# Optimization experiments

Measured on AMD Instinct MI355X. Metric: run time of the kernel, lower is better.

Reference implementation:

```python
import jax, jax.numpy as jnp
import numpy as np

B, C, H, W = 64, 256, 32, 32


def setup_inputs() -> dict:
    key = jax.random.key(0)
    ks = jax.random.split(key, 7)
    x1 = jax.random.normal(ks[0], (B, C, H, W), dtype=jnp.float32)
    x2 = jax.random.normal(ks[1], (B, C, H, W), dtype=jnp.float32)
    # 1x1 Conv2d(C+1 -> C, bias=False): weight squeezed to (C, C+1)
    conv_w = jax.random.normal(ks[2], (C, C + 1), dtype=jnp.float32) * (1.0 / np.sqrt(C + 1))
    # caLayer: Conv1d(2->4, k=1) + ReLU + Conv1d(4->1, k=1) + Softmax(dim=1)
    ca_w1 = jax.random.normal(ks[3], (4, 2), dtype=jnp.float32) * (1.0 / np.sqrt(2))
    ca_b1 = jax.random.normal(ks[4], (4,), dtype=jnp.float32) * 0.1
    ca_w2 = jax.random.normal(ks[5], (1, 4), dtype=jnp.float32) * 0.5
    ca_b2 = jax.random.normal(ks[6], (1,), dtype=jnp.float32) * 0.1
    return {"x1": x1, "x2": x2, "conv_w": conv_w, "ca_w1": ca_w1,
            "ca_b1": ca_b1, "ca_w2": ca_w2, "ca_b2": ca_b2}


def _branch_pool(x, conv_w):
    # x: (B, C, H, W)
    b, c, h, w = x.shape
    center = x[:, :, h // 2, w // 2][:, :, None, None]          # (B, C, 1, 1)
    dot = jnp.sum(x * center, axis=1, keepdims=True) / c        # (B, 1, H, W)
    concatenated = jnp.concatenate([x, dot], axis=1)            # (B, C+1, H, W)
    attn = jax.nn.sigmoid(jnp.einsum('oc,bchw->bohw', conv_w, concatenated))
    norm = attn / (jnp.sum(attn, axis=(2, 3), keepdims=True) + 1e-8)
    return jnp.sum(x * norm, axis=(2, 3))                       # (B, C)


def reference(x1, x2, conv_w, ca_w1, ca_b1, ca_w2, ca_b2):
    pooled = jnp.stack([_branch_pool(x1, conv_w),
                        _branch_pool(x2, conv_w)], axis=1)      # (B, 2, C)
    # caLayer: kernel-size-1 Conv1d == channel-mixing matmul over axis 1
    h1 = jax.nn.relu(jnp.einsum('oi,bic->boc', ca_w1, pooled) + ca_b1[None, :, None])
    h2 = jnp.einsum('oi,bic->boc', ca_w2, h1) + ca_b2[None, :, None]  # (B, 1, C)
    x_weights = jax.nn.softmax(h2, axis=1)                      # softmax over size-1 dim
    y_total = pooled * x_weights                                # broadcast (B,2,C)
    return jnp.sum(y_total, axis=1)                             # (B, C)
```

## Files before the change

kernel.cpp:

```cpp
#include <hip/hip_runtime.h>
#include <hip/hip_bf16.h>
#include <math.h>

typedef __bf16 bf16x8 __attribute__((ext_vector_type(8)));
typedef float  f32x16 __attribute__((ext_vector_type(16)));

#define WLAST_OFF 32768
#define CEN_OFF   33024
#define ACCA_OFF  65792
#define ACCX_OFF  98560

static __device__ __forceinline__ unsigned f2bf_u(float f) {
    unsigned u = __builtin_bit_cast(unsigned, f);
    return (u + 0x7fffu + ((u >> 16) & 1u)) >> 16;
}
static __device__ __forceinline__ unsigned pkbf(float a, float b) {
    __hip_bfloat162 h = __float22bfloat162_rn(make_float2(a, b));
    unsigned u; __builtin_memcpy(&u, &h, 4); return u;
}

template<int CTRL, int RM>
static __device__ __forceinline__ float dpp_add(float x) {
    int yi = __builtin_amdgcn_update_dpp(0, __builtin_bit_cast(int, x), CTRL, RM, 0xF, true);
    return x + __builtin_bit_cast(float, yi);
}
static __device__ __forceinline__ float red32(float x) {
    x = dpp_add<0x121, 0xF>(x);
    x = dpp_add<0x122, 0xF>(x);
    x = dpp_add<0x124, 0xF>(x);
    x = dpp_add<0x128, 0xF>(x);
    x = dpp_add<0x142, 0xA>(x);
    return x;
}

static __device__ __forceinline__ int swz(int hwr) {
    return ((hwr >> 2) & 7) << 2;
}

__global__ void k_init(const float* __restrict__ x1, const float* __restrict__ x2,
                       const float* __restrict__ conv_w, float* __restrict__ ws) {
    int bk = blockIdx.x;
    int tid = threadIdx.x;
    if (bk < 256) {
        int idx = bk * 256 + tid;
        int j  = idx & 7;
        int l  = (idx >> 3) & 63;
        int ot = (idx >> 9) & 7;
        int S  = idx >> 12;
        int o  = ot * 32 + (l & 31);
        int k  = S * 16 + (l >> 5) * 8 + j;
        ((unsigned short*)ws)[idx] = (unsigned short)f2bf_u(conv_w[o * 257 + k]);
        if (idx < 256) ws[WLAST_OFF + idx] = conv_w[idx * 257 + 256];
        ws[ACCA_OFF + idx] = 0.0f;
    } else {
        int xb = bk - 256;
        const float* xp = ((xb < 64) ? x1 : x2) + (size_t)(xb & 63) * (256 * 1024);
        ws[CEN_OFF + xb * 256 + tid] = xp[(size_t)tid * 1024 + 528];
    }
}

__global__ __launch_bounds__(256, 4)
void k_main(const float* __restrict__ x1, const float* __restrict__ x2,
            float* __restrict__ ws) {
    int bx = blockIdx.x;
    int xb = blockIdx.y;
    const float* xp = ((xb < 64) ? x1 : x2) + (size_t)(xb & 63) * (256 * 1024);
    const unsigned short* wfrag = (const unsigned short*)ws;
    float* accA = ws + ACCA_OFF + xb * 256;
    float* accX = ws + ACCX_OFF + xb * 256;
    int hw0 = bx * 64;

    int tid = threadIdx.x;
    int l = tid & 63, w = tid >> 6;
    int lw = l & 31, q = l >> 5;

    __shared__ unsigned sx[64][128];
    __shared__ float sd[64][17];
    __shared__ float scen[256];
    __shared__ float swl[256];
    __shared__ float dotf[64];

    int hwi = tid & 15, kc = tid >> 4;

    float cenv = ws[CEN_OFF + xb * 256 + tid];
    float wlv  = ws[WLAST_OFF + tid];
    const float* xst = xp + (size_t)(kc * 2) * 1024 + hw0 + hwi * 4;
    float4 xv[16];
    #pragma unroll
    for (int s = 0; s < 8; ++s) {
        xv[2 * s]     = *(const float4*)(xst + (size_t)(32 * s) * 1024);
        xv[2 * s + 1] = *(const float4*)(xst + (size_t)(32 * s + 1) * 1024);
    }
    __builtin_amdgcn_sched_barrier(0);
    scen[tid] = cenv;
    swl[tid]  = wlv;
    __syncthreads();

    float dotp[4] = {0.f, 0.f, 0.f, 0.f};
    #pragma unroll
    for (int s = 0; s < 8; ++s) {
        float4 e = xv[2 * s], o4 = xv[2 * s + 1];
        int c = kc * 2 + 32 * s;
        float s0 = scen[c], s1 = scen[c + 1];
        dotp[0] += e.x * s0 + o4.x * s1;
        dotp[1] += e.y * s0 + o4.y * s1;
        dotp[2] += e.z * s0 + o4.z * s1;
        dotp[3] += e.w * s0 + o4.w * s1;
        int col = kc + 16 * s;
        float ee[4] = {e.x, e.y, e.z, e.w};
        float oo[4] = {o4.x, o4.y, o4.z, o4.w};
        #pragma unroll
        for (int j = 0; j < 4; ++j) {
            int jj = (hwi + j) & 3;
            int hwr = hwi * 4 + jj;
            sx[hwr][col ^ swz(hwr)] = pkbf(ee[jj], oo[jj]);
        }
    }
    #pragma unroll
    for (int j = 0; j < 4; ++j) sd[hwi * 4 + j][kc] = dotp[j];
    __syncthreads();

    if (tid < 64) {
        float ssum = 0.f;
        #pragma unroll
        for (int k2 = 0; k2 < 16; ++k2) ssum += sd[tid][k2];
        dotf[tid] = ssum * (1.0f / 256.0f);
    }

    f32x16 acc[2][2];
    #pragma unroll
    for (int i = 0; i < 2; ++i)
        #pragma unroll
        for (int j = 0; j < 2; ++j)
            #pragma unroll
            for (int e = 0; e < 16; ++e) acc[i][j][e] = 0.0f;

    auto loadA = [&](int S, int it) -> bf16x8 {
        return *(const bf16x8*)(wfrag + (size_t)((S * 8 + (w * 2 + it)) * 64 + l) * 8);
    };
    auto loadB = [&](int S, int jt) -> bf16x8 {
        int hwr = jt * 32 + lw;
        int colb = (S * 8 + q * 4) ^ swz(hwr);
        bf16x8 r; __builtin_memcpy(&r, &sx[hwr][colb], 16);
        return r;
    };

    bf16x8 A0[2], A1[2], A2[2];
    A0[0] = loadA(0, 0); A0[1] = loadA(0, 1);
    A1[0] = loadA(1, 0); A1[1] = loadA(1, 1);
    #pragma unroll
    for (int S = 0; S < 16; ++S) {
        bf16x8 b0 = loadB(S, 0);
        bf16x8 b1 = loadB(S, 1);
        if (S + 2 < 16) { A2[0] = loadA(S + 2, 0); A2[1] = loadA(S + 2, 1); }
        acc[0][0] = __builtin_amdgcn_mfma_f32_32x32x16_bf16(A0[0], b0, acc[0][0], 0, 0, 0);
        acc[0][1] = __builtin_amdgcn_mfma_f32_32x32x16_bf16(A0[0], b1, acc[0][1], 0, 0, 0);
        acc[1][0] = __builtin_amdgcn_mfma_f32_32x32x16_bf16(A0[1], b0, acc[1][0], 0, 0, 0);
        acc[1][1] = __builtin_amdgcn_mfma_f32_32x32x16_bf16(A0[1], b1, acc[1][1], 0, 0, 0);
        A0[0] = A1[0]; A0[1] = A1[1];
        A1[0] = A2[0]; A1[1] = A2[1];
    }
    __syncthreads();

    float dv0 = dotf[lw];
    float dv1 = dotf[32 + lw];
    #pragma unroll
    for (int it = 0; it < 2; ++it) {
        int ob = w * 64 + it * 32;
        #pragma unroll
        for (int r = 0; r < 16; ++r) {
            int row = (r & 3) + 8 * (r >> 2) + 4 * q;
            int o = ob + row;
            float wl = swl[o];
            float z0 = acc[it][0][r] + wl * dv0;
            float z1 = acc[it][1][r] + wl * dv1;
            float a0 = __builtin_amdgcn_rcpf(1.0f + __expf(-z0));
            float a1 = __builtin_amdgcn_rcpf(1.0f + __expf(-z1));
            int col = o >> 1;
            unsigned w0 = sx[lw][col ^ swz(lw)];
            unsigned w1 = sx[32 + lw][col ^ swz(32 + lw)];
            float xv0, xv1;
            if (o & 1) {
                xv0 = __builtin_bit_cast(float, w0 & 0xffff0000u);
                xv1 = __builtin_bit_cast(float, w1 & 0xffff0000u);
            } else {
                xv0 = __builtin_bit_cast(float, w0 << 16);
                xv1 = __builtin_bit_cast(float, w1 << 16);
            }
            float sA = red32(a0 + a1);
            float sX = red32(a0 * xv0 + a1 * xv1);
            if (lw == 31) {
                atomicAdd(&accA[o], sA);
                atomicAdd(&accX[o], sX);
            }
        }
    }
}

__global__ void k_out(const float* __restrict__ ws, float* __restrict__ out) {
    int idx = blockIdx.x * 256 + threadIdx.x;
    int b = idx >> 8, o = idx & 255;
    float a0 = ws[ACCA_OFF + b * 256 + o];
    float p0 = ws[ACCX_OFF + b * 256 + o];
    float a1 = ws[ACCA_OFF + (64 + b) * 256 + o];
    float p1 = ws[ACCX_OFF + (64 + b) * 256 + o];
    out[idx] = p0 / (a0 + 1e-8f) + p1 / (a1 + 1e-8f);
}

extern "C" void kernel_launch(void* const* d_in, const int* in_sizes, int n_in,
                              void* d_out, int out_size, void* d_ws, size_t ws_size,
                              hipStream_t stream) {
    const float* x1     = (const float*)d_in[0];
    const float* x2     = (const float*)d_in[1];
    const float* conv_w = (const float*)d_in[2];
    float* ws  = (float*)d_ws;
    float* out = (float*)d_out;

    k_init<<<384, 256, 0, stream>>>(x1, x2, conv_w, ws);
    k_main<<<dim3(16, 128), 256, 0, stream>>>(x1, x2, ws);
    k_out<<<64, 256, 0, stream>>>(ws, out);
}
```

Measured before the change: 184.0 us.

## Split main kernel across 512 threads with per-slab LDS layout

Doubles the block to 512 threads (8 waves), so each thread loads half as many x values and each wave computes a single 32-row output tile (two MFMA accumulators instead of four). The LDS staging of x is reorganised into [S][hw][8] slabs with a simpler XOR swizzle, and the center vector is read straight from global memory instead of through shared memory. Partial dot products are reduced with wave shuffles before being written to LDS. The aim is more latency hiding and less register pressure per thread, at the cost of extra waves per block and an A-fragment prefetch depth of one.

```diff
diff --git a/kernel.cpp b/kernel.cpp
--- a/kernel.cpp
+++ b/kernel.cpp
@@ -31,10 +31,6 @@
     x = dpp_add<0x128, 0xF>(x);
     x = dpp_add<0x142, 0xA>(x);
     return x;
-}
-
-static __device__ __forceinline__ int swz(int hwr) {
-    return ((hwr >> 2) & 7) << 2;
 }
 
 __global__ void k_init(const float* __restrict__ x1, const float* __restrict__ x2,
@@ -59,7 +55,7 @@
     }
 }
 
-__global__ __launch_bounds__(256, 4)
+__global__ __launch_bounds__(512, 6)
 void k_main(const float* __restrict__ x1, const float* __restrict__ x2,
             float* __restrict__ ws) {
     int bx = blockIdx.x;
@@ -71,128 +67,123 @@
     int hw0 = bx * 64;
 
     int tid = threadIdx.x;
-    int l = tid & 63, w = tid >> 6;
+    int w = tid >> 6;
+    int l = tid & 63;
     int lw = l & 31, q = l >> 5;
 
-    __shared__ unsigned sx[64][128];
-    __shared__ float sd[64][17];
-    __shared__ float scen[256];
+    __shared__ __align__(16) unsigned sx[16][64][8];
+    __shared__ float sd[64][9];
     __shared__ float swl[256];
     __shared__ float dotf[64];
 
     int hwi = tid & 15, kc = tid >> 4;
 
-    float cenv = ws[CEN_OFF + xb * 256 + tid];
-    float wlv  = ws[WLAST_OFF + tid];
+    if (tid < 256) swl[tid] = ws[WLAST_OFF + tid];
+
+    const float* cenp = ws + CEN_OFF + xb * 256;
+    float2 cv[4];
+    #pragma unroll
+    for (int s = 0; s < 4; ++s)
+        cv[s] = *(const float2*)(cenp + kc * 2 + 64 * s);
     const float* xst = xp + (size_t)(kc * 2) * 1024 + hw0 + hwi * 4;
-    float4 xv[16];
-    #pragma unroll
-    for (int s = 0; s < 8; ++s) {
-        xv[2 * s]     = *(const float4*)(xst + (size_t)(32 * s) * 1024);
-        xv[2 * s + 1] = *(const float4*)(xst + (size_t)(32 * s + 1) * 1024);
+    float4 xv[8];
+    #pragma unroll
+    for (int s = 0; s < 4; ++s) {
+        xv[2 * s]     = *(const float4*)(xst + (size_t)(64 * s) * 1024);
+        xv[2 * s + 1] = *(const float4*)(xst + (size_t)(64 * s + 1) * 1024);
     }
     __builtin_amdgcn_sched_barrier(0);
-    scen[tid] = cenv;
-    swl[tid]  = wlv;
-    __syncthreads();
 
     float dotp[4] = {0.f, 0.f, 0.f, 0.f};
     #pragma unroll
-    for (int s = 0; s < 8; ++s) {
+    for (int s = 0; s < 4; ++s) {
         float4 e = xv[2 * s], o4 = xv[2 * s + 1];
-        int c = kc * 2 + 32 * s;
-        float s0 = scen[c], s1 = scen[c + 1];
+        float s0 = cv[s].x, s1 = cv[s].y;
         dotp[0] += e.x * s0 + o4.x * s1;
         dotp[1] += e.y * s0 + o4.y * s1;
         dotp[2] += e.z * s0 + o4.z * s1;
         dotp[3] += e.w * s0 + o4.w * s1;
-        int col = kc + 16 * s;
+        int S  = (kc >> 3) + 4 * s;
+        int wd = kc & 7;
         float ee[4] = {e.x, e.y, e.z, e.w};
         float oo[4] = {o4.x, o4.y, o4.z, o4.w};
         #pragma unroll
         for (int j = 0; j < 4; ++j) {
-            int jj = (hwi + j) & 3;
+            int jj  = (hwi + j) & 3;
             int hwr = hwi * 4 + jj;
-            sx[hwr][col ^ swz(hwr)] = pkbf(ee[jj], oo[jj]);
+            sx[S][hwr][wd ^ (((hwr >> 4) & 1) << 2)] = pkbf(ee[jj], oo[jj]);
         }
     }
     #pragma unroll
-    for (int j = 0; j < 4; ++j) sd[hwi * 4 + j][kc] = dotp[j];
+    for (int j = 0; j < 4; ++j) {
+        float v = dotp[j];
+        v += __shfl_xor(v, 16, 64);
+        v += __shfl_xor(v, 32, 64);
+        dotp[j] = v;
+    }
+    if (l < 16) {
+        #pragma unroll
+        for (int j = 0; j < 4; ++j) sd[hwi * 4 + j][w] = dotp[j];
+    }
     __syncthreads();
 
     if (tid < 64) {
         float ssum = 0.f;
         #pragma unroll
-        for (int k2 = 0; k2 < 16; ++k2) ssum += sd[tid][k2];
+        for (int k2 = 0; k2 < 8; ++k2) ssum += sd[tid][k2];
         dotf[tid] = ssum * (1.0f / 256.0f);
     }
 
-    f32x16 acc[2][2];
-    #pragma unroll
-    for (int i = 0; i < 2; ++i)
-        #pragma unroll
-        for (int j = 0; j < 2; ++j)
-            #pragma unroll
-            for (int e = 0; e < 16; ++e) acc[i][j][e] = 0.0f;
-
-    auto loadA = [&](int S, int it) -> bf16x8 {
-        return *(const bf16x8*)(wfrag + (size_t)((S * 8 + (w * 2 + it)) * 64 + l) * 8);
-    };
-    auto loadB = [&](int S, int jt) -> bf16x8 {
-        int hwr = jt * 32 + lw;
-        int colb = (S * 8 + q * 4) ^ swz(hwr);
-        bf16x8 r; __builtin_memcpy(&r, &sx[hwr][colb], 16);
-        return r;
-    };
-
-    bf16x8 A0[2], A1[2], A2[2];
-    A0[0] = loadA(0, 0); A0[1] = loadA(0, 1);
-    A1[0] = loadA(1, 0); A1[1] = loadA(1, 1);
+    f32x16 acc[2];
+    #pragma unroll
+    for (int e = 0; e < 16; ++e) { acc[0][e] = 0.0f; acc[1][e] = 0.0f; }
+
+    int sig = ((lw >> 4) & 1) << 2;
+    const unsigned* b0p = &sx[0][lw][(q * 4) ^ sig];
+    const unsigned* b1p = &sx[0][32 + lw][(q * 4) ^ sig];
+    const unsigned short* ap = wfrag + (size_t)(w * 64 + l) * 8;
+
+    bf16x8 a0 = *(const bf16x8*)(ap);
     #pragma unroll
     for (int S = 0; S < 16; ++S) {
-        bf16x8 b0 = loadB(S, 0);
-        bf16x8 b1 = loadB(S, 1);
-        if (S + 2 < 16) { A2[0] = loadA(S + 2, 0); A2[1] = loadA(S + 2, 1); }
-        acc[0][0] = __builtin_amdgcn_mfma_f32_32x32x16_bf16(A0[0], b0, acc[0][0], 0, 0, 0);
-        acc[0][1] = __builtin_amdgcn_mfma_f32_32x32x16_bf16(A0[0], b1, acc[0][1], 0, 0, 0);
-        acc[1][0] = __builtin_amdgcn_mfma_f32_32x32x16_bf16(A0[1], b0, acc[1][0], 0, 0, 0);
-        acc[1][1] = __builtin_amdgcn_mfma_f32_32x32x16_bf16(A0[1], b1, acc[1][1], 0, 0, 0);
-        A0[0] = A1[0]; A0[1] = A1[1];
-        A1[0] = A2[0]; A1[1] = A2[1];
+        bf16x8 a1;
+        if (S + 1 < 16) a1 = *(const bf16x8*)(ap + (size_t)(S + 1) * 4096);
+        bf16x8 b0, b1;
+        __builtin_memcpy(&b0, b0p + S * 512, 16);
+        __builtin_memcpy(&b1, b1p + S * 512, 16);
+        acc[0] = __builtin_amdgcn_mfma_f32_32x32x16_bf16(a0, b0, acc[0], 0, 0, 0);
+        acc[1] = __builtin_amdgcn_mfma_f32_32x32x16_bf16(a0, b1, acc[1], 0, 0, 0);
+        a0 = a1;
     }
     __syncthreads();
 
     float dv0 = dotf[lw];
     float dv1 = dotf[32 + lw];
     #pragma unroll
-    for (int it = 0; it < 2; ++it) {
-        int ob = w * 64 + it * 32;
-        #pragma unroll
-        for (int r = 0; r < 16; ++r) {
-            int row = (r & 3) + 8 * (r >> 2) + 4 * q;
-            int o = ob + row;
-            float wl = swl[o];
-            float z0 = acc[it][0][r] + wl * dv0;
-            float z1 = acc[it][1][r] + wl * dv1;
-            float a0 = __builtin_amdgcn_rcpf(1.0f + __expf(-z0));
-            float a1 = __builtin_amdgcn_rcpf(1.0f + __expf(-z1));
-            int col = o >> 1;
-            unsigned w0 = sx[lw][col ^ swz(lw)];
-            unsigned w1 = sx[32 + lw][col ^ swz(32 + lw)];
-            float xv0, xv1;
-            if (o & 1) {
-                xv0 = __builtin_bit_cast(float, w0 & 0xffff0000u);
-                xv1 = __builtin_bit_cast(float, w1 & 0xffff0000u);
-            } else {
-                xv0 = __builtin_bit_cast(float, w0 << 16);
-                xv1 = __builtin_bit_cast(float, w1 << 16);
-            }
-            float sA = red32(a0 + a1);
-            float sX = red32(a0 * xv0 + a1 * xv1);
-            if (lw == 31) {
-                atomicAdd(&accA[o], sA);
-                atomicAdd(&accX[o], sX);
-            }
+    for (int r = 0; r < 16; ++r) {
+        int row = (r & 3) + 8 * (r >> 2) + 4 * q;
+        int o = w * 32 + row;
+        float wl = swl[o];
+        float z0 = acc[0][r] + wl * dv0;
+        float z1 = acc[1][r] + wl * dv1;
+        float a0s = __builtin_amdgcn_rcpf(1.0f + __expf(-z0));
+        float a1s = __builtin_amdgcn_rcpf(1.0f + __expf(-z1));
+        int Si = o >> 4, wd = (o >> 1) & 7;
+        unsigned w0 = sx[Si][lw][wd ^ sig];
+        unsigned w1 = sx[Si][32 + lw][wd ^ sig];
+        float xv0, xv1;
+        if (o & 1) {
+            xv0 = __builtin_bit_cast(float, w0 & 0xffff0000u);
+            xv1 = __builtin_bit_cast(float, w1 & 0xffff0000u);
+        } else {
+            xv0 = __builtin_bit_cast(float, w0 << 16);
+            xv1 = __builtin_bit_cast(float, w1 << 16);
+        }
+        float sA = red32(a0s + a1s);
+        float sX = red32(a0s * xv0 + a1s * xv1);
+        if (lw == 31) {
+            atomicAdd(&accA[o], sA);
+            atomicAdd(&accX[o], sX);
         }
     }
 }
@@ -217,6 +208,6 @@
     float* out = (float*)d_out;
 
     k_init<<<384, 256, 0, stream>>>(x1, x2, conv_w, ws);
-    k_main<<<dim3(16, 128), 256, 0, stream>>>(x1, x2, ws);
+    k_main<<<dim3(16, 128), 512, 0, stream>>>(x1, x2, ws);
     k_out<<<64, 256, 0, stream>>>(ws, out);
 }
```

After: 183.0 us. Within noise of the previous version (-0.6%).
